# Kernel tuning notes

Measured on AMD Instinct MI355X. Metric: run time of the kernel, lower is better.

## Reference

```python
import jax, jax.numpy as jnp
import numpy as np

TEMPERATURE = 0.1
EPS = 1e-12  # F.normalize eps


def setup_inputs() -> dict:
    key = jax.random.key(0)
    k1, k2 = jax.random.split(key)
    B, D = 4096, 128
    return {
        "x_i": jax.random.normal(k1, (B, D), dtype=jnp.float32),
        "x_j": jax.random.normal(k2, (B, D), dtype=jnp.float32),
    }


def _l2_normalize(x):
    n = jnp.sqrt(jnp.sum(x * x, axis=1, keepdims=True))
    return x / jnp.maximum(n, EPS)


def reference(x_i, x_j):
    B = x_i.shape[0]
    z = jnp.concatenate([_l2_normalize(x_i), _l2_normalize(x_j)], axis=0)  # [2B, D]
    # cosine similarity of unit-norm rows == dot product -> single GEMM
    sim = z @ z.T  # [2B, 2B]
    idx = jnp.arange(B)
    sim_ij = sim[idx, idx + B]   # diag(sim, +B)
    sim_ji = sim[idx + B, idx]   # diag(sim, -B)
    positives = jnp.concatenate([sim_ij, sim_ji], axis=0)  # [2B]
    neg_mask = 1.0 - jnp.eye(2 * B, dtype=sim.dtype)
    denominator = jnp.sum(neg_mask * jnp.exp(sim / TEMPERATURE), axis=1)  # [2B]
    # -log(exp(pos/t) / denom) = -(pos/t - log denom)
    loss_partial = jnp.log(denominator) - positives / TEMPERATURE
    return jnp.sum(loss_partial) / (2 * B)
```

## Files before the change

kernel.cpp:

```cpp
#include <hip/hip_runtime.h>
#include <stdint.h>

#define D_DIM 128
#define NROW 8192
#define L2EPS 1e-12f
#define SCALE_PRE 0.9495707f
#define LN2 0.6931471805599453f
#define NPART 50

typedef __attribute__((ext_vector_type(4))) int   i32x4;
typedef __attribute__((ext_vector_type(8))) int   i32x8;
typedef __attribute__((ext_vector_type(4))) float f32x4;

#define AS1 __attribute__((address_space(1)))
#define AS3 __attribute__((address_space(3)))

static __device__ inline void gload_lds16(const void* g, void* l) {
    __builtin_amdgcn_global_load_lds((const AS1 uint32_t*)g, (AS3 uint32_t*)l, 16, 0, 0);
}

static __device__ inline i32x8 cat8(i32x4 lo, i32x4 hi) {
    i32x8 r;
    r[0] = lo[0]; r[1] = lo[1]; r[2] = lo[2]; r[3] = lo[3];
    r[4] = hi[0]; r[5] = hi[1]; r[6] = hi[2]; r[7] = hi[3];
    return r;
}

__global__ __launch_bounds__(256) void k_normalize(
        const float* __restrict__ xi, const float* __restrict__ xj,
        uint8_t* __restrict__ z8, float* __restrict__ pos_acc,
        float* __restrict__ logsum, unsigned* __restrict__ done_ct) {
    const int wave = threadIdx.x >> 6;
    const int lane = threadIdx.x & 63;
    const int row = blockIdx.x * 4 + wave;
    const float* src = (row < 4096) ? (xi + (size_t)row * D_DIM)
                                    : (xj + (size_t)(row - 4096) * D_DIM);
    float2 v = *(const float2*)(src + lane * 2);
    float ss = v.x * v.x + v.y * v.y;
#pragma unroll
    for (int m = 32; m >= 1; m >>= 1) ss += __shfl_xor(ss, m, 64);
    const float scale = SCALE_PRE / fmaxf(sqrtf(ss), L2EPS);
    const int pk = __builtin_amdgcn_cvt_pk_fp8_f32(v.x * scale, v.y * scale, 0, false);
    *(ushort*)(z8 + (size_t)row * D_DIM + lane * 2) = (ushort)pk;

    if (blockIdx.x == 0 && threadIdx.x == 0) {
        pos_acc[0] = 0.0f; logsum[0] = 0.0f; done_ct[0] = 0u;
    }
}

__global__ __launch_bounds__(256) void k_gemm(
        const uint8_t* __restrict__ z8, float* __restrict__ part,
        float* __restrict__ pos_acc) {
    __shared__ __align__(16) uint8_t lds[32768];

    const int t = threadIdx.x;
    const int wave = t >> 6, lane = t & 63;
    const int quad = lane >> 4, lc = lane & 15;

    const int mb = blockIdx.x >> 6;
    const int rb = blockIdx.x & 63;
    const int rowbase = rb * 128;
    const bool diag = (mb == 16);
    const int c1 = diag ? rb : (rb + 2 * mb + 1) & 63;
    const int c2 = (rb + 2 * mb + 2) & 63;

    {
        const uint8_t* zb1 = z8 + (size_t)c1 * 128 * D_DIM;
#pragma unroll
        for (int q = 0; q < 4; q++) {
            const int s = q * 256 + t;
            const int r = s >> 3;
            const int g = (s & 7) ^ (r & 7);
            gload_lds16(zb1 + (size_t)r * D_DIM + g * 16, &lds[s * 16]);
        }
        if (!diag) {
            const uint8_t* zb2 = z8 + (size_t)c2 * 128 * D_DIM;
#pragma unroll
            for (int q = 0; q < 4; q++) {
                const int s = q * 256 + t;
                const int r = s >> 3;
                const int g = (s & 7) ^ (r & 7);
                gload_lds16(zb2 + (size_t)r * D_DIM + g * 16, &lds[16384 + s * 16]);
            }
        }
    }

    i32x8 afr[2];
    {
        const uint8_t* pa = z8 + (size_t)(rowbase + wave * 32 + lc) * D_DIM + quad * 32;
#pragma unroll
        for (int i = 0; i < 2; i++) {
            i32x4 lo = *(const i32x4*)(pa + i * 16 * D_DIM);
            i32x4 hi = *(const i32x4*)(pa + i * 16 * D_DIM + 16);
            afr[i] = cat8(lo, hi);
        }
    }

    asm volatile("s_waitcnt vmcnt(0)" ::: "memory");
    __syncthreads();

    float rs[2][4] = {{0.f,0.f,0.f,0.f},{0.f,0.f,0.f,0.f}};
    float cs[16];
#pragma unroll
    for (int j = 0; j < 16; j++) cs[j] = 0.f;
    float posp = 0.f;
    const int rl0 = wave * 32 + quad * 4;

#define MFMA_J(j, A0, A1)                                                     \
    i32x4 blo, bhi; {                                                         \
        const int rowb = ((j) * 16 + lc) * D_DIM;                             \
        blo = *(const i32x4*)&lds[rowb + (((quad * 2)     ^ (lc & 7)) * 16)]; \
        bhi = *(const i32x4*)&lds[rowb + (((quad * 2 + 1) ^ (lc & 7)) * 16)]; \
    }                                                                         \
    const i32x8 bfr = cat8(blo, bhi);                                         \
    f32x4 z4 = {0.f, 0.f, 0.f, 0.f};                                          \
    f32x4 A0 = __builtin_amdgcn_mfma_scale_f32_16x16x128_f8f6f4(              \
                   afr[0], bfr, z4, 0, 0, 0, 131, 0, 127);                    \
    f32x4 A1 = __builtin_amdgcn_mfma_scale_f32_16x16x128_f8f6f4(              \
                   afr[1], bfr, z4, 0, 0, 0, 131, 0, 127);

    if (!diag) {
#pragma unroll
        for (int j = 0; j < 8; j++) {
            MFMA_J(j, a0, a1)
#pragma unroll
            for (int r = 0; r < 4; r++) {
                const float e0 = exp2f(a0[r]);
                const float e1 = exp2f(a1[r]);
                rs[0][r] += e0;
                rs[1][r] += e1;
                cs[j] += e0 + e1;
            }
        }
        if (mb < 15) {
#pragma unroll
            for (int j = 8; j < 16; j++) {
                MFMA_J(j, a0, a1)
#pragma unroll
                for (int r = 0; r < 4; r++) {
                    const float e0 = exp2f(a0[r]);
                    const float e1 = exp2f(a1[r]);
                    rs[0][r] += e0;
                    rs[1][r] += e1;
                    cs[j] += e0 + e1;
                }
            }
        } else {
#pragma unroll
            for (int j = 8; j < 16; j++) {
                MFMA_J(j, a0, a1)
                const int clb = (j - 8) * 16 + lc;
#pragma unroll
                for (int i = 0; i < 2; i++)
#pragma unroll
                    for (int r = 0; r < 4; r++) {
                        const float s = (i ? a1 : a0)[r];
                        const float e = 0.5f * exp2f(s);
                        if (clb == rl0 + i * 16 + r) posp += s;
                        rs[i][r] += e;
                        cs[j] += e;
                    }
            }
        }
    } else {
#pragma unroll
        for (int j = 0; j < 8; j++) {
            MFMA_J(j, a0, a1)
            const int cl = j * 16 + lc;
#pragma unroll
            for (int i = 0; i < 2; i++)
#pragma unroll
                for (int r = 0; r < 4; r++) {
                    const float s = (i ? a1 : a0)[r];
                    const float e = (cl > rl0 + i * 16 + r) ? exp2f(s) : 0.f;
                    rs[i][r] += e;
                    cs[j] += e;
                }
        }
    }
#undef MFMA_J

#pragma unroll
    for (int i = 0; i < 2; i++)
#pragma unroll
        for (int r = 0; r < 4; r++) {
            float v = rs[i][r];
            v += __shfl_xor(v, 1, 64);
            v += __shfl_xor(v, 2, 64);
            v += __shfl_xor(v, 4, 64);
            v += __shfl_xor(v, 8, 64);
            if (lc == 0)
                part[(size_t)mb * NROW + rowbase + rl0 + i * 16 + r] = v;
        }

#pragma unroll
    for (int j = 0; j < 16; j++) {
        cs[j] += __shfl_xor(cs[j], 16, 64);
        cs[j] += __shfl_xor(cs[j], 32, 64);
    }
    __syncthreads();
    float* colred = (float*)lds;
    if (quad == 0) {
#pragma unroll
        for (int j = 0; j < 16; j++)
            colred[wave * 256 + j * 16 + lc] = cs[j];
    }
    __syncthreads();
    if (t < 256) {
        const float v = colred[t] + colred[256 + t] + colred[512 + t] + colred[768 + t];
        if (!diag) {
            const int slot = 17 + 2 * mb + (t >> 7);
            const int band = (t < 128) ? c1 : c2;
            part[(size_t)slot * NROW + band * 128 + (t & 127)] = v;
        } else if (t < 128) {
            part[(size_t)49 * NROW + c1 * 128 + t] = v;
        }
    }

    if (mb == 15) {
#pragma unroll
        for (int mm = 32; mm >= 1; mm >>= 1) posp += __shfl_xor(posp, mm, 64);
        if (lane == 0) atomicAdd(pos_acc, posp);
    }
}

__global__ __launch_bounds__(256) void k_logsum(
        const float* __restrict__ part, float* __restrict__ pos_acc,
        float* __restrict__ logsum, unsigned* __restrict__ done_ct,
        float* __restrict__ out) {
    const int row = blockIdx.x * 256 + threadIdx.x;
    float d = 0.f;
#pragma unroll
    for (int p = 0; p < NPART; p++) d += part[(size_t)p * NROW + row];
    float v = __logf(d);
#pragma unroll
    for (int m = 32; m >= 1; m >>= 1) v += __shfl_xor(v, m, 64);
    if ((threadIdx.x & 63) == 0) atomicAdd(logsum, v);
    __threadfence();
    __syncthreads();
    if (threadIdx.x == 0) {
        const unsigned prev = atomicAdd(done_ct, 1u);
        if (prev == gridDim.x - 1) {
            __threadfence();
            const float ls = atomicAdd(logsum, 0.0f);
            const float pp = atomicAdd(pos_acc, 0.0f);
            out[0] = (ls - pp * LN2) / (float)NROW;
        }
    }
}

extern "C" void kernel_launch(void* const* d_in, const int* in_sizes, int n_in,
                              void* d_out, int out_size, void* d_ws, size_t ws_size,
                              hipStream_t stream) {
    const float* xi = (const float*)d_in[0];
    const float* xj = (const float*)d_in[1];
    uint8_t* z8 = (uint8_t*)d_ws;
    float* part = (float*)(z8 + (size_t)NROW * D_DIM);
    float* pos_acc = part + (size_t)NPART * NROW;
    float* logsum = pos_acc + 1;
    unsigned* done_ct = (unsigned*)(logsum + 1);
    float* out = (float*)d_out;

    hipLaunchKernelGGL(k_normalize, dim3(NROW / 4), dim3(256), 0, stream,
                       xi, xj, z8, pos_acc, logsum, done_ct);
    hipLaunchKernelGGL(k_gemm, dim3(17 * 64), dim3(256), 0, stream,
                       z8, part, pos_acc);
    hipLaunchKernelGGL(k_logsum, dim3(NROW / 256), dim3(256), 0, stream,
                       part, pos_acc, logsum, done_ct, out);
}
```

Baseline: 84.17 us.

## Make GEMM blocks persistent over multiple tiles with double-buffered LDS staging

```diff
diff --git a/kernel.cpp b/kernel.cpp
--- a/kernel.cpp
+++ b/kernel.cpp
@@ -6,7 +6,7 @@
 #define L2EPS 1e-12f
 #define SCALE_PRE 0.9495707f
 #define LN2 0.6931471805599453f
-#define NPART 50
+#define NPART 149
 
 typedef __attribute__((ext_vector_type(4))) int   i32x4;
 typedef __attribute__((ext_vector_type(8))) int   i32x8;
@@ -17,6 +17,12 @@
 
 static __device__ inline void gload_lds16(const void* g, void* l) {
     __builtin_amdgcn_global_load_lds((const AS1 uint32_t*)g, (AS3 uint32_t*)l, 16, 0, 0);
+}
+
+static __device__ __forceinline__ void memfence_barrier() {
+    asm volatile("" ::: "memory");
+    __builtin_amdgcn_s_barrier();
+    asm volatile("" ::: "memory");
 }
 
 static __device__ inline i32x8 cat8(i32x4 lo, i32x4 hi) {
@@ -48,69 +54,49 @@
     }
 }
 
-__global__ __launch_bounds__(256) void k_gemm(
-        const uint8_t* __restrict__ z8, float* __restrict__ part,
-        float* __restrict__ pos_acc) {
-    __shared__ __align__(16) uint8_t lds[32768];
-
-    const int t = threadIdx.x;
-    const int wave = t >> 6, lane = t & 63;
-    const int quad = lane >> 4, lc = lane & 15;
-
-    const int mb = blockIdx.x >> 6;
-    const int rb = blockIdx.x & 63;
-    const int rowbase = rb * 128;
+static __device__ __forceinline__ void stage_tile(
+        const uint8_t* __restrict__ z8, uint8_t* dst, int mb, int rb, int t) {
+    const int c1 = (mb == 16) ? rb : (rb + 2 * mb + 1) & 63;
+    const int c2 = (mb == 16) ? rb : (rb + 2 * mb + 2) & 63;
+    const uint8_t* zb1 = z8 + (size_t)c1 * 128 * D_DIM;
+    const uint8_t* zb2 = z8 + (size_t)c2 * 128 * D_DIM;
+#pragma unroll
+    for (int q = 0; q < 4; q++) {
+        const int s = q * 256 + t;
+        const int r = s >> 3;
+        const int g = (s & 7) ^ (r & 7);
+        gload_lds16(zb1 + (size_t)r * D_DIM + g * 16, dst + s * 16);
+    }
+#pragma unroll
+    for (int q = 0; q < 4; q++) {
+        const int s = q * 256 + t;
+        const int r = s >> 3;
+        const int g = (s & 7) ^ (r & 7);
+        gload_lds16(zb2 + (size_t)r * D_DIM + g * 16, dst + 16384 + s * 16);
+    }
+}
+
+static __device__ __forceinline__ void compute_tile(
+        const uint8_t* __restrict__ buf, int mb, int rb,
+        int wave, int lane, int quad, int lc, const i32x8* afr,
+        float* __restrict__ part, float* __restrict__ pos_acc) {
     const bool diag = (mb == 16);
     const int c1 = diag ? rb : (rb + 2 * mb + 1) & 63;
     const int c2 = (rb + 2 * mb + 2) & 63;
-
-    {
-        const uint8_t* zb1 = z8 + (size_t)c1 * 128 * D_DIM;
-#pragma unroll
-        for (int q = 0; q < 4; q++) {
-            const int s = q * 256 + t;
-            const int r = s >> 3;
-            const int g = (s & 7) ^ (r & 7);
-            gload_lds16(zb1 + (size_t)r * D_DIM + g * 16, &lds[s * 16]);
-        }
-        if (!diag) {
-            const uint8_t* zb2 = z8 + (size_t)c2 * 128 * D_DIM;
-#pragma unroll
-            for (int q = 0; q < 4; q++) {
-                const int s = q * 256 + t;
-                const int r = s >> 3;
-                const int g = (s & 7) ^ (r & 7);
-                gload_lds16(zb2 + (size_t)r * D_DIM + g * 16, &lds[16384 + s * 16]);
-            }
-        }
-    }
-
-    i32x8 afr[2];
-    {
-        const uint8_t* pa = z8 + (size_t)(rowbase + wave * 32 + lc) * D_DIM + quad * 32;
-#pragma unroll
-        for (int i = 0; i < 2; i++) {
-            i32x4 lo = *(const i32x4*)(pa + i * 16 * D_DIM);
-            i32x4 hi = *(const i32x4*)(pa + i * 16 * D_DIM + 16);
-            afr[i] = cat8(lo, hi);
-        }
-    }
-
-    asm volatile("s_waitcnt vmcnt(0)" ::: "memory");
-    __syncthreads();
+    const int rowbase = rb * 128;
+    const int rl0 = wave * 32 + quad * 4;
 
     float rs[2][4] = {{0.f,0.f,0.f,0.f},{0.f,0.f,0.f,0.f}};
     float cs[16];
 #pragma unroll
     for (int j = 0; j < 16; j++) cs[j] = 0.f;
     float posp = 0.f;
-    const int rl0 = wave * 32 + quad * 4;
 
 #define MFMA_J(j, A0, A1)                                                     \
     i32x4 blo, bhi; {                                                         \
         const int rowb = ((j) * 16 + lc) * D_DIM;                             \
-        blo = *(const i32x4*)&lds[rowb + (((quad * 2)     ^ (lc & 7)) * 16)]; \
-        bhi = *(const i32x4*)&lds[rowb + (((quad * 2 + 1) ^ (lc & 7)) * 16)]; \
+        blo = *(const i32x4*)&buf[rowb + (((quad * 2)     ^ (lc & 7)) * 16)]; \
+        bhi = *(const i32x4*)&buf[rowb + (((quad * 2 + 1) ^ (lc & 7)) * 16)]; \
     }                                                                         \
     const i32x8 bfr = cat8(blo, bhi);                                         \
     f32x4 z4 = {0.f, 0.f, 0.f, 0.f};                                          \
@@ -193,27 +179,23 @@
                 part[(size_t)mb * NROW + rowbase + rl0 + i * 16 + r] = v;
         }
 
-#pragma unroll
-    for (int j = 0; j < 16; j++) {
+    const int njc = diag ? 8 : 16;
+    for (int j = 0; j < njc; j++) {
         cs[j] += __shfl_xor(cs[j], 16, 64);
         cs[j] += __shfl_xor(cs[j], 32, 64);
     }
-    __syncthreads();
-    float* colred = (float*)lds;
     if (quad == 0) {
-#pragma unroll
-        for (int j = 0; j < 16; j++)
-            colred[wave * 256 + j * 16 + lc] = cs[j];
-    }
-    __syncthreads();
-    if (t < 256) {
-        const float v = colred[t] + colred[256 + t] + colred[512 + t] + colred[768 + t];
         if (!diag) {
-            const int slot = 17 + 2 * mb + (t >> 7);
-            const int band = (t < 128) ? c1 : c2;
-            part[(size_t)slot * NROW + band * 128 + (t & 127)] = v;
-        } else if (t < 128) {
-            part[(size_t)49 * NROW + c1 * 128 + t] = v;
+#pragma unroll
+            for (int j = 0; j < 8; j++)
+                part[(size_t)(17 + mb * 8 + wave * 2) * NROW + c1 * 128 + j * 16 + lc] = cs[j];
+#pragma unroll
+            for (int j = 8; j < 16; j++)
+                part[(size_t)(17 + mb * 8 + wave * 2 + 1) * NROW + c2 * 128 + (j - 8) * 16 + lc] = cs[j];
+        } else {
+#pragma unroll
+            for (int j = 0; j < 8; j++)
+                part[(size_t)(145 + wave) * NROW + c1 * 128 + j * 16 + lc] = cs[j];
         }
     }
 
@@ -221,6 +203,55 @@
 #pragma unroll
         for (int mm = 32; mm >= 1; mm >>= 1) posp += __shfl_xor(posp, mm, 64);
         if (lane == 0) atomicAdd(pos_acc, posp);
+    }
+}
+
+__global__ __launch_bounds__(256) void k_gemm(
+        const uint8_t* __restrict__ z8, float* __restrict__ part,
+        float* __restrict__ pos_acc) {
+    __shared__ __align__(16) uint8_t lds[2][32768];
+
+    const int t = threadIdx.x;
+    const int wave = t >> 6, lane = t & 63;
+    const int quad = lane >> 4, lc = lane & 15;
+
+    const int b = blockIdx.x;
+    const int rb = b & 63;
+    const int mb0 = b >> 6;
+    const int nt = (b < 64) ? 3 : 2;
+    const int rowbase = rb * 128;
+
+    i32x8 afr[2];
+    {
+        const uint8_t* pa = z8 + (size_t)(rowbase + wave * 32 + lc) * D_DIM + quad * 32;
+#pragma unroll
+        for (int i = 0; i < 2; i++) {
+            i32x4 lo = *(const i32x4*)(pa + i * 16 * D_DIM);
+            i32x4 hi = *(const i32x4*)(pa + i * 16 * D_DIM + 16);
+            afr[i] = cat8(lo, hi);
+        }
+    }
+
+    stage_tile(z8, lds[0], mb0, rb, t);
+    stage_tile(z8, lds[1], mb0 + 8, rb, t);
+    asm volatile("s_waitcnt vmcnt(8)" ::: "memory");
+    memfence_barrier();
+
+    for (int tt = 0; tt < nt; tt++) {
+        const int mb = (tt == 2) ? 16 : mb0 + 8 * tt;
+        compute_tile(lds[tt & 1], mb, rb, wave, lane, quad, lc, afr,
+                     part, pos_acc);
+        if (tt + 2 < nt) {
+            memfence_barrier();
+            stage_tile(z8, lds[tt & 1], 16, rb, t);
+        }
+        if (tt + 1 < nt) {
+            if (tt + 2 < nt)
+                asm volatile("s_waitcnt vmcnt(8)" ::: "memory");
+            else
+                asm volatile("s_waitcnt vmcnt(0)" ::: "memory");
+            memfence_barrier();
+        }
     }
 }
 
@@ -230,7 +261,6 @@
         float* __restrict__ out) {
     const int row = blockIdx.x * 256 + threadIdx.x;
     float d = 0.f;
-#pragma unroll
     for (int p = 0; p < NPART; p++) d += part[(size_t)p * NROW + row];
     float v = __logf(d);
 #pragma unroll
@@ -263,7 +293,7 @@
 
     hipLaunchKernelGGL(k_normalize, dim3(NROW / 4), dim3(256), 0, stream,
                        xi, xj, z8, pos_acc, logsum, done_ct);
-    hipLaunchKernelGGL(k_gemm, dim3(17 * 64), dim3(256), 0, stream,
+    hipLaunchKernelGGL(k_gemm, dim3(512), dim3(256), 0, stream,
                        z8, part, pos_acc);
     hipLaunchKernelGGL(k_logsum, dim3(NROW / 256), dim3(256), 0, stream,
                        part, pos_acc, logsum, done_ct, out);
```

Measured after the change: 109.5 us. 1.3x slower.
